# Optimization experiments

Hardware: AMD Instinct MI355X
Metric: run time of the kernel (lower is better)

The kernel has to match this reference:

```python
import jax, jax.numpy as jnp
import numpy as np

N_NODES = 100000
N_EDGES = 1600000
H, D, DE = 4, 32, 32  # heads, node_out_feats, edge_out_feats
NEG_SLOPE = 0.2


def setup_inputs() -> dict:
    key = jax.random.key(0)
    ks = jax.random.split(key, 10)
    return {
        "node_inputs": jax.random.normal(ks[0], (N_NODES, 128), jnp.float32),
        "edge_inputs": jax.random.normal(ks[1], (N_EDGES, 16), jnp.float32),
        "src": jax.random.randint(ks[2], (N_EDGES,), 0, N_NODES, jnp.int32),
        "dst": jax.random.randint(ks[3], (N_EDGES,), 0, N_NODES, jnp.int32),
        "W_fc": jax.random.normal(ks[4], (128, H * D), jnp.float32) * 0.1,
        "attn_src_p": jax.random.normal(ks[5], (1, H, D), jnp.float32) * 0.1,
        "attn_dst_p": jax.random.normal(ks[6], (1, H, D), jnp.float32) * 0.1,
        "W_edge": jax.random.normal(ks[7], (16, H * DE), jnp.float32) * 0.1,
        "attn_edge_p": jax.random.normal(ks[8], (1, H, DE), jnp.float32) * 0.1,
        "W_res": jax.random.normal(ks[9], (128, H * D), jnp.float32) * 0.1,
        "bias_p": jnp.zeros((H * D,), jnp.float32),
    }


def reference(node_inputs, edge_inputs, src, dst, W_fc, attn_src_p,
              attn_dst_p, W_edge, attn_edge_p, W_res, bias_p):
    N = node_inputs.shape[0]
    # node projection: [N, H, D]
    feat = (node_inputs @ W_fc).reshape(N, H, D)
    # per-node attention logits [N, H]
    a_src = (feat * attn_src_p).sum(-1)
    a_dst = (feat * attn_dst_p).sum(-1)
    # edge-feature attention logits [E, H]
    feat_e = (edge_inputs @ W_edge).reshape(-1, H, DE)
    a_edge = (feat_e * attn_edge_p).sum(-1)
    # per-edge score: u_add_v + edge term, then LeakyReLU
    e = a_src[src] + a_dst[dst] + a_edge                 # [E, H]
    e = jnp.where(e > 0, e, NEG_SLOPE * e)
    # edge softmax grouped by destination node
    emax = jax.lax.stop_gradient(jax.ops.segment_max(e, dst, num_segments=N))
    ex = jnp.exp(e - emax[dst])
    denom = jax.ops.segment_sum(ex, dst, num_segments=N)
    attn = ex / denom[dst]                               # [E, H]
    # weighted scatter-aggregate of source features
    msg = feat[src] * attn[:, :, None]                   # [E, H, D]
    x = jax.ops.segment_sum(msg, dst, num_segments=N)    # [N, H, D]
    # residual + bias
    x = x + (node_inputs @ W_res).reshape(N, H, D)
    x = x + bias_p.reshape(H, D)
    return x
```

## Files before the change

### kernel.cpp

```cpp
#include <hip/hip_runtime.h>
#include <math.h>

#define NNODES_FEAT 128
#define HD 128
#define H 4
#define D 32
#define EDGE_F 16
#define NEG_SLOPE 0.2f

typedef _Float16 f16;
typedef _Float16 f16x2 __attribute__((ext_vector_type(2)));
typedef _Float16 f16x4 __attribute__((ext_vector_type(4)));
typedef _Float16 f16x8 __attribute__((ext_vector_type(8)));
typedef float f32x4 __attribute__((ext_vector_type(4)));

union ExPack { float2 f; f16x4 h; };

__global__ void k_wedge(const float* __restrict__ W_edge,
                        const float* __restrict__ attn_edge,
                        float* __restrict__ w_eh) {
    int t = threadIdx.x;
    int k = t >> 2;
    int h = t & 3;
    float s = 0.f;
    for (int d = 0; d < D; ++d)
        s += W_edge[k * HD + h * D + d] * attn_edge[h * D + d];
    w_eh[k * H + h] = s;
}

__global__ __launch_bounds__(256) void k_wt(const float* __restrict__ Wfc,
                                            const float* __restrict__ Wres,
                                            f16* __restrict__ Wt) {
    int i = blockIdx.x * 256 + threadIdx.x;
    int n = i >> 7, k = i & 127;
    float v = (n < 128) ? Wfc[k * HD + n] : Wres[k * HD + (n - 128)];
    Wt[(size_t)n * 128 + k] = (f16)v;
}

#define LDK 136
__global__ __launch_bounds__(256) void k_gemm_mfma(
    const float* __restrict__ A, const f16* __restrict__ Wt,
    const float* __restrict__ bias, f16* __restrict__ feat16,
    float* __restrict__ out, int N) {
    __shared__ f16 As[64 * LDK];
    __shared__ f16 Bs[128 * LDK];
    int tid = threadIdx.x;
    int wave = tid >> 6, lane = tid & 63;
    int m0 = blockIdx.x * 64;
    int cb = blockIdx.y;

    for (int c = tid; c < 64 * 32; c += 256) {
        int r = c >> 5, cc = (c & 31) * 4;
        int gr = m0 + r;
        float4 v = make_float4(0.f, 0.f, 0.f, 0.f);
        if (gr < N) v = *(const float4*)(A + (size_t)gr * 128 + cc);
        f16x4 h = {(f16)v.x, (f16)v.y, (f16)v.z, (f16)v.w};
        *(f16x4*)(&As[r * LDK + cc]) = h;
    }
    const f16* Wblk = Wt + (size_t)cb * 128 * 128;
    for (int c = tid; c < 128 * 16; c += 256) {
        int r = c >> 4, cc = (c & 15) * 8;
        float4 v = *(const float4*)(Wblk + (size_t)r * 128 + cc);
        *(float4*)(&Bs[r * LDK + cc]) = v;
    }
    __syncthreads();

    int am = lane & 15, aq = lane >> 4;
    f32x4 acc[8];
#pragma unroll
    for (int nt = 0; nt < 8; ++nt) acc[nt] = (f32x4){0.f, 0.f, 0.f, 0.f};

    int arow = wave * 16 + am;
#pragma unroll
    for (int kc = 0; kc < 4; ++kc) {
        f16x8 a = *(const f16x8*)(&As[arow * LDK + kc * 32 + aq * 8]);
#pragma unroll
        for (int nt = 0; nt < 8; ++nt) {
            f16x8 b = *(const f16x8*)(&Bs[(nt * 16 + am) * LDK + kc * 32 + aq * 8]);
            acc[nt] = __builtin_amdgcn_mfma_f32_16x16x32_f16(a, b, acc[nt], 0, 0, 0);
        }
    }

    int orow0 = m0 + wave * 16 + aq * 4;
    if (cb == 0) {
#pragma unroll
        for (int nt = 0; nt < 8; ++nt) {
            int col = nt * 16 + am;
#pragma unroll
            for (int r = 0; r < 4; ++r) {
                int row = orow0 + r;
                if (row < N) feat16[(size_t)row * 128 + col] = (f16)acc[nt][r];
            }
        }
    } else {
#pragma unroll
        for (int nt = 0; nt < 8; ++nt) {
            int col = nt * 16 + am;
            float bv = bias[col];
#pragma unroll
            for (int r = 0; r < 4; ++r) {
                int row = orow0 + r;
                if (row < N) out[(size_t)row * 128 + col] = acc[nt][r] + bv;
            }
        }
    }
}

__global__ __launch_bounds__(256) void k_attn_nodes(
    const f16* __restrict__ feat16, const float* __restrict__ attn_src,
    const float* __restrict__ attn_dst, float* __restrict__ a_src,
    float* __restrict__ a_dst, int N) {
    int g = blockIdx.x * 256 + threadIdx.x;
    int n = g >> 2, h = g & 3;
    if (n >= N) return;
    const f16* f = feat16 + (size_t)n * HD + h * D;
    const float* w1 = attn_src + h * D;
    const float* w2 = attn_dst + h * D;
    float s1 = 0.f, s2 = 0.f;
#pragma unroll
    for (int d = 0; d < D; d += 2) {
        f16x2 fv = *(const f16x2*)(f + d);
        float f0 = (float)fv.x, f1 = (float)fv.y;
        s1 += f0 * w1[d] + f1 * w1[d + 1];
        s2 += f0 * w2[d] + f1 * w2[d + 1];
    }
    a_src[n * H + h] = s1;
    a_dst[n * H + h] = s2;
}

__global__ __launch_bounds__(256) void k_count(const int* __restrict__ dst,
                                               int* __restrict__ deg,
                                               int* __restrict__ rank, int E) {
    int base = blockIdx.x * 1024 + threadIdx.x;
#pragma unroll
    for (int j = 0; j < 4; ++j) {
        int e = base + j * 256;
        if (e < E) rank[e] = atomicAdd(deg + dst[e], 1);
    }
}

__global__ __launch_bounds__(256) void k_scan_partial(
    const int* __restrict__ deg, int* __restrict__ partial, int N) {
    __shared__ int sdata[256];
    int t = threadIdx.x;
    int base = blockIdx.x * 1024 + t * 4;
    int s = 0;
#pragma unroll
    for (int j = 0; j < 4; ++j) { int i = base + j; if (i < N) s += deg[i]; }
    sdata[t] = s;
    __syncthreads();
    for (int off = 128; off > 0; off >>= 1) {
        if (t < off) sdata[t] += sdata[t + off];
        __syncthreads();
    }
    if (t == 0) partial[blockIdx.x] = sdata[0];
}

__global__ __launch_bounds__(256) void k_scan_top(
    int* __restrict__ partial, int* __restrict__ offs, int nb, int N) {
    __shared__ int sdata[256];
    int t = threadIdx.x;
    int v = (t < nb) ? partial[t] : 0;
    sdata[t] = v;
    __syncthreads();
    for (int off = 1; off < 256; off <<= 1) {
        int add = (t >= off) ? sdata[t - off] : 0;
        __syncthreads();
        sdata[t] += add;
        __syncthreads();
    }
    int excl = (t == 0) ? 0 : sdata[t - 1];
    if (t < nb) partial[t] = excl;
    if (t == nb - 1) offs[N] = sdata[t];
}

__global__ __launch_bounds__(256) void k_scan_final(
    int* __restrict__ deg_offs, const int* __restrict__ partial, int N) {
    __shared__ int sdata[256];
    int t = threadIdx.x;
    int base = blockIdx.x * 1024 + t * 4;
    int v[4]; int s = 0;
#pragma unroll
    for (int j = 0; j < 4; ++j) { int i = base + j; v[j] = (i < N) ? deg_offs[i] : 0; s += v[j]; }
    sdata[t] = s;
    __syncthreads();
    for (int off = 1; off < 256; off <<= 1) {
        int add = (t >= off) ? sdata[t - off] : 0;
        __syncthreads();
        sdata[t] += add;
        __syncthreads();
    }
    int excl = partial[blockIdx.x] + ((t == 0) ? 0 : sdata[t - 1]);
#pragma unroll
    for (int j = 0; j < 4; ++j) {
        int i = base + j;
        if (i < N) { deg_offs[i] = excl; excl += v[j]; }
    }
}

__global__ __launch_bounds__(256) void k_edge_fill(
    const float* __restrict__ edge_inputs, const int* __restrict__ src,
    const int* __restrict__ dst, const float* __restrict__ w_eh,
    const float* __restrict__ a_src, const float* __restrict__ a_dst,
    const int* __restrict__ offs, const int* __restrict__ rank,
    float4* __restrict__ rec, int E) {
    __shared__ float weh_s[EDGE_F * H];
    if (threadIdx.x < EDGE_F * H) weh_s[threadIdx.x] = w_eh[threadIdx.x];
    __syncthreads();

    int base = blockIdx.x * 1024 + threadIdx.x;

    int sj[4], dj[4], rj[4];
    bool valid[4];
#pragma unroll
    for (int j = 0; j < 4; ++j) {
        int e = base + j * 256;
        valid[j] = (e < E);
        sj[j] = valid[j] ? src[e] : 0;
        dj[j] = valid[j] ? dst[e] : 0;
        rj[j] = valid[j] ? rank[e] : 0;
    }

    float4 as[4], ad[4];
    int pos[4];
#pragma unroll
    for (int j = 0; j < 4; ++j) {
        as[j] = *(const float4*)(a_src + sj[j] * H);
        ad[j] = *(const float4*)(a_dst + dj[j] * H);
        pos[j] = offs[dj[j]] + rj[j];
    }

#pragma unroll
    for (int j = 0; j < 4; ++j) {
        if (!valid[j]) continue;
        int e = base + j * 256;
        const float* x = edge_inputs + (size_t)e * EDGE_F;
        float4 x0 = *(const float4*)(x);
        float4 x1 = *(const float4*)(x + 4);
        float4 x2 = *(const float4*)(x + 8);
        float4 x3 = *(const float4*)(x + 12);
        float xs[16] = {x0.x, x0.y, x0.z, x0.w, x1.x, x1.y, x1.z, x1.w,
                        x2.x, x2.y, x2.z, x2.w, x3.x, x3.y, x3.z, x3.w};
        float ae0 = 0.f, ae1 = 0.f, ae2 = 0.f, ae3 = 0.f;
#pragma unroll
        for (int k = 0; k < EDGE_F; ++k) {
            float xv = xs[k];
            ae0 += xv * weh_s[k * H + 0];
            ae1 += xv * weh_s[k * H + 1];
            ae2 += xv * weh_s[k * H + 2];
            ae3 += xv * weh_s[k * H + 3];
        }
        float ev[H];
        ev[0] = as[j].x + ad[j].x + ae0;
        ev[1] = as[j].y + ad[j].y + ae1;
        ev[2] = as[j].z + ad[j].z + ae2;
        ev[3] = as[j].w + ad[j].w + ae3;
#pragma unroll
        for (int h = 0; h < H; ++h) {
            float t = ev[h];
            t = t > 0.f ? t : NEG_SLOPE * t;
            ev[h] = __expf(t);
        }
        ExPack p;
        p.h = (f16x4){(f16)ev[0], (f16)ev[1], (f16)ev[2], (f16)ev[3]};
        float4 r;
        r.x = __int_as_float(sj[j]);
        r.y = p.f.x;
        r.z = p.f.y;
        r.w = 0.f;
        rec[pos[j]] = r;
    }
}

__global__ __launch_bounds__(256) void k_aggr(
    const f16* __restrict__ feat16, const float4* __restrict__ rec,
    const int* __restrict__ offs, float* __restrict__ out, int N) {
    int wave = threadIdx.x >> 6;
    int lane = threadIdx.x & 63;
    int n = blockIdx.x * 4 + wave;
    if (n >= N) return;
    int beg = offs[n], end = offs[n + 1];
    if (end <= beg) return;
    int h = lane >> 4;
    size_t c0 = (size_t)2 * lane;
    float num0 = 0.f, num1 = 0.f, den = 0.f;
    int i = beg;
    for (; i + 3 < end; i += 4) {
        float4 r0 = rec[i], r1 = rec[i + 1], r2 = rec[i + 2], r3 = rec[i + 3];
        int s0 = __float_as_int(r0.x), s1 = __float_as_int(r1.x);
        int s2 = __float_as_int(r2.x), s3 = __float_as_int(r3.x);
        f16x2 f0 = *(const f16x2*)(feat16 + (size_t)s0 * HD + c0);
        f16x2 f1 = *(const f16x2*)(feat16 + (size_t)s1 * HD + c0);
        f16x2 f2 = *(const f16x2*)(feat16 + (size_t)s2 * HD + c0);
        f16x2 f3 = *(const f16x2*)(feat16 + (size_t)s3 * HD + c0);
        ExPack p0, p1, p2, p3;
        p0.f = make_float2(r0.y, r0.z);
        p1.f = make_float2(r1.y, r1.z);
        p2.f = make_float2(r2.y, r2.z);
        p3.f = make_float2(r3.y, r3.z);
        float e0 = (float)p0.h[h], e1 = (float)p1.h[h];
        float e2 = (float)p2.h[h], e3 = (float)p3.h[h];
        num0 += e0 * (float)f0.x + e1 * (float)f1.x + e2 * (float)f2.x + e3 * (float)f3.x;
        num1 += e0 * (float)f0.y + e1 * (float)f1.y + e2 * (float)f2.y + e3 * (float)f3.y;
        den += e0 + e1 + e2 + e3;
    }
    for (; i < end; ++i) {
        float4 r0 = rec[i];
        int s0 = __float_as_int(r0.x);
        f16x2 f0 = *(const f16x2*)(feat16 + (size_t)s0 * HD + c0);
        ExPack p0;
        p0.f = make_float2(r0.y, r0.z);
        float e0 = (float)p0.h[h];
        num0 += e0 * (float)f0.x;
        num1 += e0 * (float)f0.y;
        den += e0;
    }
    float inv = 1.f / den;
    size_t o = (size_t)n * HD + c0;
    float2 v = *(float2*)(out + o);
    v.x += num0 * inv;
    v.y += num1 * inv;
    *(float2*)(out + o) = v;
}

extern "C" void kernel_launch(void* const* d_in, const int* in_sizes, int n_in,
                              void* d_out, int out_size, void* d_ws, size_t ws_size,
                              hipStream_t stream) {
    const float* node_inputs = (const float*)d_in[0];
    const float* edge_inputs = (const float*)d_in[1];
    const int*   src         = (const int*)d_in[2];
    const int*   dst         = (const int*)d_in[3];
    const float* W_fc        = (const float*)d_in[4];
    const float* attn_src_p  = (const float*)d_in[5];
    const float* attn_dst_p  = (const float*)d_in[6];
    const float* W_edge      = (const float*)d_in[7];
    const float* attn_edge_p = (const float*)d_in[8];
    const float* W_res       = (const float*)d_in[9];
    const float* bias_p      = (const float*)d_in[10];

    int N = in_sizes[0] / NNODES_FEAT;
    int E = in_sizes[2];

    float* out = (float*)d_out;

    f16*    feat16  = (f16*)d_ws;
    float4* rec     = (float4*)(feat16 + (size_t)N * HD);
    f16*    Wt      = (f16*)(rec + (size_t)E);
    float*  a_src   = (float*)(Wt + 256 * 128);
    float*  a_dst   = a_src + (size_t)N * H;
    float*  w_eh    = a_dst + (size_t)N * H;
    int*    deg     = (int*)(w_eh + 64);
    int*    offs    = deg;
    int*    partial = deg + (N + 2);
    int*    rank    = partial + 128;

    hipMemsetAsync(deg, 0, (size_t)(N + 2) * sizeof(int), stream);

    k_wedge<<<1, 64, 0, stream>>>(W_edge, attn_edge_p, w_eh);
    k_wt<<<(256 * 128) / 256, 256, 0, stream>>>(W_fc, W_res, Wt);

    dim3 g1((N + 63) / 64, 2);
    k_gemm_mfma<<<g1, 256, 0, stream>>>(node_inputs, Wt, bias_p, feat16, out, N);

    int nb = (N * H + 255) / 256;
    k_attn_nodes<<<nb, 256, 0, stream>>>(feat16, attn_src_p, attn_dst_p, a_src, a_dst, N);

    int eb = (E + 1023) / 1024;
    k_count<<<eb, 256, 0, stream>>>(dst, deg, rank, E);
    int sb = (N + 1023) / 1024;
    k_scan_partial<<<sb, 256, 0, stream>>>(deg, partial, N);
    k_scan_top<<<1, 256, 0, stream>>>(partial, offs, sb, N);
    k_scan_final<<<sb, 256, 0, stream>>>(deg, partial, N);

    k_edge_fill<<<eb, 256, 0, stream>>>(edge_inputs, src, dst, w_eh, a_src, a_dst,
                                        offs, rank, rec, E);

    int ab = (N + 3) / 4;
    k_aggr<<<ab, 256, 0, stream>>>(feat16, rec, offs, out, N);
}
```

Measured before the change: 504.9 us.

## Move edge MLP into count kernel, merge GEMM column blocks, cheaper half extraction

The edge-feature attention projection moves from the edge-fill kernel into the atomic degree-count kernel. The aim is to hide the latency of the dst atomics behind the edge_inputs loads and FMA work, and to leave edge_fill as a lighter scatter pass. The result is passed on as a packed fp16 per-edge buffer, which adds an extra write and read of E*8 bytes. The GEMM now covers both weight halves in one block with a 1D grid, so each A tile is converted once, at the cost of half as many blocks. In aggregation, the per-head fp16 exp value is pulled out with a select and shift instead of dynamic vector indexing.

```diff
diff --git a/kernel.cpp b/kernel.cpp
--- a/kernel.cpp
+++ b/kernel.cpp
@@ -47,7 +47,6 @@
     int tid = threadIdx.x;
     int wave = tid >> 6, lane = tid & 63;
     int m0 = blockIdx.x * 64;
-    int cb = blockIdx.y;
 
     for (int c = tid; c < 64 * 32; c += 256) {
         int r = c >> 5, cc = (c & 31) * 4;
@@ -57,50 +56,54 @@
         f16x4 h = {(f16)v.x, (f16)v.y, (f16)v.z, (f16)v.w};
         *(f16x4*)(&As[r * LDK + cc]) = h;
     }
-    const f16* Wblk = Wt + (size_t)cb * 128 * 128;
-    for (int c = tid; c < 128 * 16; c += 256) {
-        int r = c >> 4, cc = (c & 15) * 8;
-        float4 v = *(const float4*)(Wblk + (size_t)r * 128 + cc);
-        *(float4*)(&Bs[r * LDK + cc]) = v;
-    }
-    __syncthreads();
 
     int am = lane & 15, aq = lane >> 4;
-    f32x4 acc[8];
-#pragma unroll
-    for (int nt = 0; nt < 8; ++nt) acc[nt] = (f32x4){0.f, 0.f, 0.f, 0.f};
-
     int arow = wave * 16 + am;
-#pragma unroll
-    for (int kc = 0; kc < 4; ++kc) {
-        f16x8 a = *(const f16x8*)(&As[arow * LDK + kc * 32 + aq * 8]);
-#pragma unroll
-        for (int nt = 0; nt < 8; ++nt) {
-            f16x8 b = *(const f16x8*)(&Bs[(nt * 16 + am) * LDK + kc * 32 + aq * 8]);
-            acc[nt] = __builtin_amdgcn_mfma_f32_16x16x32_f16(a, b, acc[nt], 0, 0, 0);
-        }
-    }
-
     int orow0 = m0 + wave * 16 + aq * 4;
-    if (cb == 0) {
-#pragma unroll
-        for (int nt = 0; nt < 8; ++nt) {
-            int col = nt * 16 + am;
-#pragma unroll
-            for (int r = 0; r < 4; ++r) {
-                int row = orow0 + r;
-                if (row < N) feat16[(size_t)row * 128 + col] = (f16)acc[nt][r];
+
+    for (int cb = 0; cb < 2; ++cb) {
+        if (cb) __syncthreads();
+        const f16* Wblk = Wt + (size_t)cb * 128 * 128;
+        for (int c = tid; c < 128 * 16; c += 256) {
+            int r = c >> 4, cc = (c & 15) * 8;
+            float4 v = *(const float4*)(Wblk + (size_t)r * 128 + cc);
+            *(float4*)(&Bs[r * LDK + cc]) = v;
+        }
+        __syncthreads();
+
+        f32x4 acc[8];
+#pragma unroll
+        for (int nt = 0; nt < 8; ++nt) acc[nt] = (f32x4){0.f, 0.f, 0.f, 0.f};
+#pragma unroll
+        for (int kc = 0; kc < 4; ++kc) {
+            f16x8 a = *(const f16x8*)(&As[arow * LDK + kc * 32 + aq * 8]);
+#pragma unroll
+            for (int nt = 0; nt < 8; ++nt) {
+                f16x8 b = *(const f16x8*)(&Bs[(nt * 16 + am) * LDK + kc * 32 + aq * 8]);
+                acc[nt] = __builtin_amdgcn_mfma_f32_16x16x32_f16(a, b, acc[nt], 0, 0, 0);
             }
         }
-    } else {
-#pragma unroll
-        for (int nt = 0; nt < 8; ++nt) {
-            int col = nt * 16 + am;
-            float bv = bias[col];
-#pragma unroll
-            for (int r = 0; r < 4; ++r) {
-                int row = orow0 + r;
-                if (row < N) out[(size_t)row * 128 + col] = acc[nt][r] + bv;
+
+        if (cb == 0) {
+#pragma unroll
+            for (int nt = 0; nt < 8; ++nt) {
+                int col = nt * 16 + am;
+#pragma unroll
+                for (int r = 0; r < 4; ++r) {
+                    int row = orow0 + r;
+                    if (row < N) feat16[(size_t)row * 128 + col] = (f16)acc[nt][r];
+                }
+            }
+        } else {
+#pragma unroll
+            for (int nt = 0; nt < 8; ++nt) {
+                int col = nt * 16 + am;
+                float bv = bias[col];
+#pragma unroll
+                for (int r = 0; r < 4; ++r) {
+                    int row = orow0 + r;
+                    if (row < N) out[(size_t)row * 128 + col] = acc[nt][r] + bv;
+                }
             }
         }
     }
@@ -128,14 +131,67 @@
     a_dst[n * H + h] = s2;
 }
 
-__global__ __launch_bounds__(256) void k_count(const int* __restrict__ dst,
-                                               int* __restrict__ deg,
-                                               int* __restrict__ rank, int E) {
-    int base = blockIdx.x * 1024 + threadIdx.x;
-#pragma unroll
-    for (int j = 0; j < 4; ++j) {
-        int e = base + j * 256;
-        if (e < E) rank[e] = atomicAdd(deg + dst[e], 1);
+__global__ __launch_bounds__(256) void k_count_mlp(
+    const float* __restrict__ edge_inputs, const int* __restrict__ dst,
+    const float* __restrict__ w_eh, int* __restrict__ deg,
+    int* __restrict__ rank, float2* __restrict__ ae16, int E) {
+    __shared__ float weh_s[EDGE_F * H];
+    if (threadIdx.x < EDGE_F * H) weh_s[threadIdx.x] = w_eh[threadIdx.x];
+    __syncthreads();
+
+    int base = blockIdx.x * 512 + threadIdx.x;
+    int e0 = base, e1 = base + 256;
+    bool v0 = e0 < E, v1 = e1 < E;
+
+    int d0 = v0 ? dst[e0] : 0;
+    int d1 = v1 ? dst[e1] : 0;
+
+    float4 xa[4], xb[4];
+    if (v0) {
+        const float* x = edge_inputs + (size_t)e0 * EDGE_F;
+        xa[0] = *(const float4*)(x);      xa[1] = *(const float4*)(x + 4);
+        xa[2] = *(const float4*)(x + 8);  xa[3] = *(const float4*)(x + 12);
+    }
+    if (v1) {
+        const float* x = edge_inputs + (size_t)e1 * EDGE_F;
+        xb[0] = *(const float4*)(x);      xb[1] = *(const float4*)(x + 4);
+        xb[2] = *(const float4*)(x + 8);  xb[3] = *(const float4*)(x + 12);
+    }
+
+    int r0 = v0 ? atomicAdd(deg + d0, 1) : 0;
+    int r1 = v1 ? atomicAdd(deg + d1, 1) : 0;
+
+    if (v0) {
+        float ae0 = 0.f, ae1 = 0.f, ae2 = 0.f, ae3 = 0.f;
+        const float* xs = (const float*)xa;
+#pragma unroll
+        for (int k = 0; k < EDGE_F; ++k) {
+            float xv = xs[k];
+            ae0 += xv * weh_s[k * H + 0];
+            ae1 += xv * weh_s[k * H + 1];
+            ae2 += xv * weh_s[k * H + 2];
+            ae3 += xv * weh_s[k * H + 3];
+        }
+        ExPack p;
+        p.h = (f16x4){(f16)ae0, (f16)ae1, (f16)ae2, (f16)ae3};
+        ae16[e0] = p.f;
+        rank[e0] = r0;
+    }
+    if (v1) {
+        float ae0 = 0.f, ae1 = 0.f, ae2 = 0.f, ae3 = 0.f;
+        const float* xs = (const float*)xb;
+#pragma unroll
+        for (int k = 0; k < EDGE_F; ++k) {
+            float xv = xs[k];
+            ae0 += xv * weh_s[k * H + 0];
+            ae1 += xv * weh_s[k * H + 1];
+            ae2 += xv * weh_s[k * H + 2];
+            ae3 += xv * weh_s[k * H + 3];
+        }
+        ExPack p;
+        p.h = (f16x4){(f16)ae0, (f16)ae1, (f16)ae2, (f16)ae3};
+        ae16[e1] = p.f;
+        rank[e1] = r1;
     }
 }
 
@@ -199,62 +255,34 @@
 }
 
 __global__ __launch_bounds__(256) void k_edge_fill(
-    const float* __restrict__ edge_inputs, const int* __restrict__ src,
-    const int* __restrict__ dst, const float* __restrict__ w_eh,
+    const int* __restrict__ src, const int* __restrict__ dst,
+    const int* __restrict__ rank, const float2* __restrict__ ae16,
     const float* __restrict__ a_src, const float* __restrict__ a_dst,
-    const int* __restrict__ offs, const int* __restrict__ rank,
-    float4* __restrict__ rec, int E) {
-    __shared__ float weh_s[EDGE_F * H];
-    if (threadIdx.x < EDGE_F * H) weh_s[threadIdx.x] = w_eh[threadIdx.x];
-    __syncthreads();
-
-    int base = blockIdx.x * 1024 + threadIdx.x;
-
-    int sj[4], dj[4], rj[4];
-    bool valid[4];
-#pragma unroll
-    for (int j = 0; j < 4; ++j) {
-        int e = base + j * 256;
-        valid[j] = (e < E);
-        sj[j] = valid[j] ? src[e] : 0;
-        dj[j] = valid[j] ? dst[e] : 0;
-        rj[j] = valid[j] ? rank[e] : 0;
-    }
-
-    float4 as[4], ad[4];
-    int pos[4];
-#pragma unroll
-    for (int j = 0; j < 4; ++j) {
-        as[j] = *(const float4*)(a_src + sj[j] * H);
-        ad[j] = *(const float4*)(a_dst + dj[j] * H);
-        pos[j] = offs[dj[j]] + rj[j];
-    }
-
-#pragma unroll
-    for (int j = 0; j < 4; ++j) {
-        if (!valid[j]) continue;
-        int e = base + j * 256;
-        const float* x = edge_inputs + (size_t)e * EDGE_F;
-        float4 x0 = *(const float4*)(x);
-        float4 x1 = *(const float4*)(x + 4);
-        float4 x2 = *(const float4*)(x + 8);
-        float4 x3 = *(const float4*)(x + 12);
-        float xs[16] = {x0.x, x0.y, x0.z, x0.w, x1.x, x1.y, x1.z, x1.w,
-                        x2.x, x2.y, x2.z, x2.w, x3.x, x3.y, x3.z, x3.w};
-        float ae0 = 0.f, ae1 = 0.f, ae2 = 0.f, ae3 = 0.f;
-#pragma unroll
-        for (int k = 0; k < EDGE_F; ++k) {
-            float xv = xs[k];
-            ae0 += xv * weh_s[k * H + 0];
-            ae1 += xv * weh_s[k * H + 1];
-            ae2 += xv * weh_s[k * H + 2];
-            ae3 += xv * weh_s[k * H + 3];
-        }
+    const int* __restrict__ offs, float4* __restrict__ rec, int E) {
+    int base = blockIdx.x * 512 + threadIdx.x;
+    int e0 = base, e1 = base + 256;
+    bool v0 = e0 < E, v1 = e1 < E;
+
+    int s0 = v0 ? src[e0] : 0, s1 = v1 ? src[e1] : 0;
+    int d0 = v0 ? dst[e0] : 0, d1 = v1 ? dst[e1] : 0;
+    int r0 = v0 ? rank[e0] : 0, r1 = v1 ? rank[e1] : 0;
+    float2 q0 = v0 ? ae16[e0] : make_float2(0.f, 0.f);
+    float2 q1 = v1 ? ae16[e1] : make_float2(0.f, 0.f);
+
+    float4 as0 = *(const float4*)(a_src + s0 * H);
+    float4 as1 = *(const float4*)(a_src + s1 * H);
+    float4 ad0 = *(const float4*)(a_dst + d0 * H);
+    float4 ad1 = *(const float4*)(a_dst + d1 * H);
+    int p0 = offs[d0] + r0;
+    int p1 = offs[d1] + r1;
+
+    if (v0) {
+        ExPack qa; qa.f = q0;
         float ev[H];
-        ev[0] = as[j].x + ad[j].x + ae0;
-        ev[1] = as[j].y + ad[j].y + ae1;
-        ev[2] = as[j].z + ad[j].z + ae2;
-        ev[3] = as[j].w + ad[j].w + ae3;
+        ev[0] = as0.x + ad0.x + (float)qa.h[0];
+        ev[1] = as0.y + ad0.y + (float)qa.h[1];
+        ev[2] = as0.z + ad0.z + (float)qa.h[2];
+        ev[3] = as0.w + ad0.w + (float)qa.h[3];
 #pragma unroll
         for (int h = 0; h < H; ++h) {
             float t = ev[h];
@@ -264,12 +292,42 @@
         ExPack p;
         p.h = (f16x4){(f16)ev[0], (f16)ev[1], (f16)ev[2], (f16)ev[3]};
         float4 r;
-        r.x = __int_as_float(sj[j]);
+        r.x = __int_as_float(s0);
         r.y = p.f.x;
         r.z = p.f.y;
         r.w = 0.f;
-        rec[pos[j]] = r;
-    }
+        rec[p0] = r;
+    }
+    if (v1) {
+        ExPack qa; qa.f = q1;
+        float ev[H];
+        ev[0] = as1.x + ad1.x + (float)qa.h[0];
+        ev[1] = as1.y + ad1.y + (float)qa.h[1];
+        ev[2] = as1.z + ad1.z + (float)qa.h[2];
+        ev[3] = as1.w + ad1.w + (float)qa.h[3];
+#pragma unroll
+        for (int h = 0; h < H; ++h) {
+            float t = ev[h];
+            t = t > 0.f ? t : NEG_SLOPE * t;
+            ev[h] = __expf(t);
+        }
+        ExPack p;
+        p.h = (f16x4){(f16)ev[0], (f16)ev[1], (f16)ev[2], (f16)ev[3]};
+        float4 r;
+        r.x = __int_as_float(s1);
+        r.y = p.f.x;
+        r.z = p.f.y;
+        r.w = 0.f;
+        rec[p1] = r;
+    }
+}
+
+__device__ __forceinline__ float exsel(float a, float b, int hword, int hshift) {
+    unsigned u = __float_as_uint(hword ? b : a);
+    unsigned short us = (unsigned short)(u >> hshift);
+    f16 hv;
+    __builtin_memcpy(&hv, &us, 2);
+    return (float)hv;
 }
 
 __global__ __launch_bounds__(256) void k_aggr(
@@ -281,7 +339,8 @@
     if (n >= N) return;
     int beg = offs[n], end = offs[n + 1];
     if (end <= beg) return;
-    int h = lane >> 4;
+    int hword = (lane >> 5) & 1;
+    int hshift = ((lane >> 4) & 1) * 16;
     size_t c0 = (size_t)2 * lane;
     float num0 = 0.f, num1 = 0.f, den = 0.f;
     int i = beg;
@@ -293,13 +352,10 @@
         f16x2 f1 = *(const f16x2*)(feat16 + (size_t)s1 * HD + c0);
         f16x2 f2 = *(const f16x2*)(feat16 + (size_t)s2 * HD + c0);
         f16x2 f3 = *(const f16x2*)(feat16 + (size_t)s3 * HD + c0);
-        ExPack p0, p1, p2, p3;
-        p0.f = make_float2(r0.y, r0.z);
-        p1.f = make_float2(r1.y, r1.z);
-        p2.f = make_float2(r2.y, r2.z);
-        p3.f = make_float2(r3.y, r3.z);
-        float e0 = (float)p0.h[h], e1 = (float)p1.h[h];
-        float e2 = (float)p2.h[h], e3 = (float)p3.h[h];
+        float e0 = exsel(r0.y, r0.z, hword, hshift);
+        float e1 = exsel(r1.y, r1.z, hword, hshift);
+        float e2 = exsel(r2.y, r2.z, hword, hshift);
+        float e3 = exsel(r3.y, r3.z, hword, hshift);
         num0 += e0 * (float)f0.x + e1 * (float)f1.x + e2 * (float)f2.x + e3 * (float)f3.x;
         num1 += e0 * (float)f0.y + e1 * (float)f1.y + e2 * (float)f2.y + e3 * (float)f3.y;
         den += e0 + e1 + e2 + e3;
@@ -308,9 +364,7 @@
         float4 r0 = rec[i];
         int s0 = __float_as_int(r0.x);
         f16x2 f0 = *(const f16x2*)(feat16 + (size_t)s0 * HD + c0);
-        ExPack p0;
-        p0.f = make_float2(r0.y, r0.z);
-        float e0 = (float)p0.h[h];
+        float e0 = exsel(r0.y, r0.z, hword, hshift);
         num0 += e0 * (float)f0.x;
         num1 += e0 * (float)f0.y;
         den += e0;
@@ -353,27 +407,28 @@
     int*    offs    = deg;
     int*    partial = deg + (N + 2);
     int*    rank    = partial + 128;
+    float2* ae16    = (float2*)(rank + (size_t)E);
 
     hipMemsetAsync(deg, 0, (size_t)(N + 2) * sizeof(int), stream);
 
     k_wedge<<<1, 64, 0, stream>>>(W_edge, attn_edge_p, w_eh);
     k_wt<<<(256 * 128) / 256, 256, 0, stream>>>(W_fc, W_res, Wt);
 
-    dim3 g1((N + 63) / 64, 2);
-    k_gemm_mfma<<<g1, 256, 0, stream>>>(node_inputs, Wt, bias_p, feat16, out, N);
+    int gb = (N + 63) / 64;
+    k_gemm_mfma<<<gb, 256, 0, stream>>>(node_inputs, Wt, bias_p, feat16, out, N);
 
     int nb = (N * H + 255) / 256;
     k_attn_nodes<<<nb, 256, 0, stream>>>(feat16, attn_src_p, attn_dst_p, a_src, a_dst, N);
 
-    int eb = (E + 1023) / 1024;
-    k_count<<<eb, 256, 0, stream>>>(dst, deg, rank, E);
+    int eb = (E + 511) / 512;
+    k_count_mlp<<<eb, 256, 0, stream>>>(edge_inputs, dst, w_eh, deg, rank, ae16, E);
     int sb = (N + 1023) / 1024;
     k_scan_partial<<<sb, 256, 0, stream>>>(deg, partial, N);
     k_scan_top<<<1, 256, 0, stream>>>(partial, offs, sb, N);
     k_scan_final<<<sb, 256, 0, stream>>>(deg, partial, N);
 
-    k_edge_fill<<<eb, 256, 0, stream>>>(edge_inputs, src, dst, w_eh, a_src, a_dst,
-                                        offs, rank, rec, E);
+    k_edge_fill<<<eb, 256, 0, stream>>>(src, dst, rank, ae16, a_src, a_dst,
+                                        offs, rec, E);
 
     int ab = (N + 3) / 4;
     k_aggr<<<ab, 256, 0, stream>>>(feat16, rec, offs, out, N);
```

New measurement: 455.5 us. -9.8%, faster.
